# Performance work log

Measured on AMD Instinct MI355X. Metric: run time of the kernel, lower is better.

The kernel has to match this reference:

```python
import jax, jax.numpy as jnp
import numpy as np

HEADS = 8


def setup_inputs() -> dict:
    key = jax.random.key(0)
    k0, k1, k2, k3 = jax.random.split(key, 4)
    N, C_in, T = 4, 256, 2048
    C_kq, C_out = 512, 512
    x = jax.random.normal(k0, (N, C_in, T), dtype=jnp.float32)
    # Conv1d(kernel_size=1, bias=False) weights squeezed to (out, in)
    Wq = jax.random.normal(k1, (C_kq, C_in), dtype=jnp.float32) * 0.02
    Wk = jax.random.normal(k2, (C_kq, C_in), dtype=jnp.float32) * 0.02
    Wv = jax.random.normal(k3, (C_out, C_in), dtype=jnp.float32) * 0.02
    return {"x": x, "Wq": Wq, "Wk": Wk, "Wv": Wv}


def reference(x, Wq, Wk, Wv):
    N, C, T = x.shape
    H = HEADS
    C_kq = Wq.shape[0]
    C_out = Wv.shape[0]
    dk = C_kq // H
    dv = C_out // H
    # 1x1 conv == per-timestep linear projection
    q = jnp.einsum('oc,nct->not', Wq, x).reshape(N, H, dk, T)
    k = jnp.einsum('oc,nct->not', Wk, x).reshape(N, H, dk, T)
    v = jnp.einsum('oc,nct->not', Wv, x).reshape(N, H, dv, T)
    scale = 1.0 / np.sqrt(dk)
    # scores[n,h,tk,tq] = sum_d q[n,h,d,tq] * k[n,h,d,tk]
    scores = jnp.einsum('nhdq,nhdk->nhkq', q, k) * scale
    attn = jax.nn.softmax(scores, axis=2)  # softmax over key axis tk
    # out[n,h,d,tq] = sum_tk attn[n,h,tk,tq] * v[n,h,d,tk]
    out = jnp.einsum('nhkq,nhdk->nhdq', attn, v)
    return out.reshape(N, C_out, T)
```

## Files before the change

kernel.cpp:

```cpp
#include <hip/hip_runtime.h>
#include <stdint.h>

#define T_SEQ 2048
#define CIN 256
#define COUT 512
#define NHEAD 8
#define DH 64
#define LROW 72

typedef __bf16 bf16x8 __attribute__((ext_vector_type(8)));
typedef float f32x4 __attribute__((ext_vector_type(4)));
typedef float f32x16 __attribute__((ext_vector_type(16)));
typedef unsigned short u16x8 __attribute__((ext_vector_type(8)));
typedef unsigned u32x4 __attribute__((ext_vector_type(4)));

static __device__ __forceinline__ unsigned short bf16_rne(float f) {
  unsigned u = __builtin_bit_cast(unsigned, f);
  u += 0x7FFFu + ((u >> 16) & 1u);
  return (unsigned short)(u >> 16);
}

static __device__ __forceinline__ unsigned cvt_pk_bf16(float lo, float hi) {
  unsigned r;
  asm("v_cvt_pk_bf16_f32 %0, %1, %2" : "=v"(r) : "v"(lo), "v"(hi));
  return r;
}

static __device__ __forceinline__ void plswap(unsigned& a, unsigned& b) {
  auto rr = __builtin_amdgcn_permlane32_swap((int)a, (int)b, false, false);
  a = (unsigned)rr[0];
  b = (unsigned)rr[1];
}

static __device__ __forceinline__ bf16x8 ld_frag(const unsigned short* p) {
  u16x8 v = *(const u16x8*)p;
  return __builtin_bit_cast(bf16x8, v);
}

__global__ __launch_bounds__(256) void pack_k(const float* __restrict__ x,
                                              const float* __restrict__ wq,
                                              const float* __restrict__ wk,
                                              const float* __restrict__ wv,
                                              unsigned short* __restrict__ wb,
                                              unsigned short* __restrict__ xT) {
  __shared__ float tile[64][65];
  const int b = blockIdx.x;
  const int i = threadIdx.x;
  if (b < 1536) {
    const int idx = b * 256 + i;
    const float* src = (idx < 131072) ? wq : (idx < 262144) ? wk : wv;
    wb[idx] = bf16_rne(src[idx & 131071]);
    return;
  }
  const int b2 = b - 1536;
  const int t0 = (b2 & 31) * 64, c0 = ((b2 >> 5) & 3) * 64, n = b2 >> 7;
  {
    const int cc = i >> 2, tch = (i & 3) * 16;
    const float* src = x + ((size_t)n * CIN + c0 + cc) * T_SEQ + t0 + tch;
    const float4* s4 = (const float4*)src;
#pragma unroll
    for (int q = 0; q < 4; ++q) {
      float4 v = s4[q];
      tile[cc][tch + q * 4 + 0] = v.x;
      tile[cc][tch + q * 4 + 1] = v.y;
      tile[cc][tch + q * 4 + 2] = v.z;
      tile[cc][tch + q * 4 + 3] = v.w;
    }
  }
  __syncthreads();
  {
    const int tt = i >> 2, cch = (i & 3) * 16;
    unsigned short* dst = xT + ((size_t)n * T_SEQ + t0 + tt) * CIN + c0 + cch;
    u16x8 w0, w1;
#pragma unroll
    for (int j = 0; j < 8; ++j) w0[j] = bf16_rne(tile[cch + j][tt]);
#pragma unroll
    for (int j = 0; j < 8; ++j) w1[j] = bf16_rne(tile[cch + 8 + j][tt]);
    *(u16x8*)dst = w0;
    *(u16x8*)(dst + 8) = w1;
  }
}

__global__ __launch_bounds__(256) void proj_k(const unsigned short* __restrict__ wb,
                                              const unsigned short* __restrict__ xT,
                                              unsigned short* __restrict__ qb,
                                              unsigned short* __restrict__ kb,
                                              unsigned short* __restrict__ vb) {
  __shared__ unsigned short vt_lds[64][136];
  const int n = blockIdx.z;
  const unsigned short* X = xT + (size_t)n * T_SEQ * CIN;
  const int tid = threadIdx.x, wave = tid >> 6, lane = tid & 63;
  const int c = lane & 15, g = lane >> 4;
  const int o0 = blockIdx.x * 64;
  const int t0 = blockIdx.y * 128 + wave * 32;

  bf16x8 a[8][2];
#pragma unroll
  for (int k8 = 0; k8 < 8; ++k8)
#pragma unroll
    for (int mt = 0; mt < 2; ++mt)
      a[k8][mt] = ld_frag(X + (size_t)(t0 + mt * 16 + c) * CIN + k8 * 32 + g * 8);

  const f32x4 z4 = {0.f, 0.f, 0.f, 0.f};
  const int h = o0 >> 6;
  const size_t base = ((size_t)(n * NHEAD + h)) * T_SEQ * DH;

  for (int w = 0; w < 3; ++w) {
    const unsigned short* W = wb + (size_t)w * COUT * CIN;
    f32x4 acc[2][4];
#pragma unroll
    for (int mt = 0; mt < 2; ++mt)
#pragma unroll
      for (int no = 0; no < 4; ++no) acc[mt][no] = z4;

#pragma unroll
    for (int k8 = 0; k8 < 8; ++k8) {
      bf16x8 b[4];
#pragma unroll
      for (int no = 0; no < 4; ++no)
        b[no] = ld_frag(W + (size_t)(o0 + no * 16 + c) * CIN + k8 * 32 + g * 8);
#pragma unroll
      for (int mt = 0; mt < 2; ++mt)
#pragma unroll
        for (int no = 0; no < 4; ++no)
          acc[mt][no] = __builtin_amdgcn_mfma_f32_16x16x32_bf16(a[k8][mt], b[no], acc[mt][no], 0, 0, 0);
    }

    if (w == 2) {
#pragma unroll
      for (int mt = 0; mt < 2; ++mt)
#pragma unroll
        for (int no = 0; no < 4; ++no) {
          const int d = no * 16 + c;
          const int lt = (wave * 32) + mt * 16 + 4 * g;
#pragma unroll
          for (int pr = 0; pr < 2; ++pr) {
            const unsigned pw = (unsigned)bf16_rne(acc[mt][no][2 * pr]) |
                                ((unsigned)bf16_rne(acc[mt][no][2 * pr + 1]) << 16);
            *(unsigned*)&vt_lds[d][lt + 2 * pr] = pw;
          }
        }
      __syncthreads();
      const int row = tid >> 2, seg = tid & 3;
      unsigned short* dst = vb + base + (size_t)row * T_SEQ + blockIdx.y * 128 + seg * 32;
      const unsigned short* srcl = &vt_lds[row][seg * 32];
#pragma unroll
      for (int q = 0; q < 4; ++q) *(u16x8*)(dst + q * 8) = *(const u16x8*)(srcl + q * 8);
    } else {
      unsigned short* dst = (w == 0) ? qb : kb;
      const float scale = (w == 0) ? 0.18033688011112043f : 1.0f;
#pragma unroll
      for (int mt = 0; mt < 2; ++mt)
#pragma unroll
        for (int no = 0; no < 4; ++no)
#pragma unroll
          for (int r = 0; r < 4; ++r) {
            const int t = t0 + mt * 16 + 4 * g + r;
            const int d = no * 16 + c;
            dst[base + (size_t)t * DH + d] = bf16_rne(acc[mt][no][r] * scale);
          }
    }
  }
}

__global__ __launch_bounds__(256) void attn_k(const unsigned short* __restrict__ qb,
                                              const unsigned short* __restrict__ kb,
                                              const unsigned short* __restrict__ vbt,
                                              float* __restrict__ outp) {
  __shared__ unsigned short smem[4 * 4608];
  unsigned short* kA = smem;
  unsigned short* kB = smem + 4608;
  unsigned short* vA = smem + 9216;
  unsigned short* vB = smem + 13824;

  const int bid = blockIdx.x;
  const int sid = (bid & 7) * 32 + (bid >> 3);
  const int tqt = sid & 7, nh = sid >> 3;

  const int tid = threadIdx.x;
  const int lane = tid & 63;
  const int wave = tid >> 6;
  const int ln = lane & 31, hi = lane >> 5;
  const int tq0 = tqt * 256 + wave * 64;
  const unsigned short* Q = qb + (size_t)nh * T_SEQ * DH;
  const unsigned short* K = kb + (size_t)nh * T_SEQ * DH;
  const unsigned short* V = vbt + (size_t)nh * T_SEQ * DH;

  bf16x8 qf0[4], qf1[4];
#pragma unroll
  for (int dblk = 0; dblk < 4; ++dblk) {
    qf0[dblk] = ld_frag(Q + (size_t)(tq0 + ln) * DH + dblk * 16 + hi * 8);
    qf1[dblk] = ld_frag(Q + (size_t)(tq0 + 32 + ln) * DH + dblk * 16 + hi * 8);
  }

  const f32x16 z16 = {0.f, 0.f, 0.f, 0.f, 0.f, 0.f, 0.f, 0.f,
                      0.f, 0.f, 0.f, 0.f, 0.f, 0.f, 0.f, 0.f};
  f32x16 oacc00 = z16, oacc01 = z16, oacc10 = z16, oacc11 = z16;
  float l_run0 = 0.f, l_run1 = 0.f;

  const int srow = tid & 63, sseg = tid >> 6;
  const unsigned short* kseg = K + (size_t)srow * DH + sseg * 16;
  const unsigned short* vseg = V + (size_t)srow * T_SEQ + sseg * 16;
  const int swoff = srow * LROW + sseg * 16;
  const int row0 = ln * LROW;
  const int row1 = (32 + ln) * LROW;
  const int hioff = hi * 8;

  const int NT = T_SEQ / 64;
  u16x8 kn0, kn1, vn0, vn1;

  {
    u16x8 a0 = *(const u16x8*)kseg;
    u16x8 a1 = *(const u16x8*)(kseg + 8);
    u16x8 b0 = *(const u16x8*)vseg;
    u16x8 b1 = *(const u16x8*)(vseg + 8);
    *(u16x8*)&kA[swoff] = a0;
    *(u16x8*)&kA[swoff + 8] = a1;
    *(u16x8*)&vA[swoff] = b0;
    *(u16x8*)&vA[swoff + 8] = b1;
    kn0 = *(const u16x8*)(kseg + 64 * DH);
    kn1 = *(const u16x8*)(kseg + 64 * DH + 8);
  }
  __syncthreads();

  f32x16 sa[4], sb[4];
  {
    __builtin_amdgcn_s_setprio(1);
#pragma unroll
    for (int dblk = 0; dblk < 4; ++dblk) {
      bf16x8 ka0 = ld_frag(kA + row0 + dblk * 16 + hioff);
      bf16x8 ka1 = ld_frag(kA + row1 + dblk * 16 + hioff);
      sa[0] = __builtin_amdgcn_mfma_f32_32x32x16_bf16(ka0, qf0[dblk], (dblk == 0) ? z16 : sa[0], 0, 0, 0);
      sa[1] = __builtin_amdgcn_mfma_f32_32x32x16_bf16(ka1, qf0[dblk], (dblk == 0) ? z16 : sa[1], 0, 0, 0);
      sa[2] = __builtin_amdgcn_mfma_f32_32x32x16_bf16(ka0, qf1[dblk], (dblk == 0) ? z16 : sa[2], 0, 0, 0);
      sa[3] = __builtin_amdgcn_mfma_f32_32x32x16_bf16(ka1, qf1[dblk], (dblk == 0) ? z16 : sa[3], 0, 0, 0);
    }
    __builtin_amdgcn_s_setprio(0);
  }
  *(u16x8*)&kB[swoff] = kn0;
  *(u16x8*)&kB[swoff + 8] = kn1;
  kn0 = *(const u16x8*)(kseg + 2 * 64 * DH);
  kn1 = *(const u16x8*)(kseg + 2 * 64 * DH + 8);
  vn0 = *(const u16x8*)(vseg + 64);
  vn1 = *(const u16x8*)(vseg + 64 + 8);
  __syncthreads();

  auto body = [&](int t, f32x16 (&sc)[4], f32x16 (&sn)[4],
                  unsigned short* krd, unsigned short* kwr,
                  unsigned short* vrd, unsigned short* vwr) {
    const bool qn = (t + 1 < NT);
    if (qn) {
      __builtin_amdgcn_s_setprio(1);
#pragma unroll
      for (int dblk = 0; dblk < 4; ++dblk) {
        bf16x8 ka0 = ld_frag(krd + row0 + dblk * 16 + hioff);
        bf16x8 ka1 = ld_frag(krd + row1 + dblk * 16 + hioff);
        sn[0] = __builtin_amdgcn_mfma_f32_32x32x16_bf16(ka0, qf0[dblk], (dblk == 0) ? z16 : sn[0], 0, 0, 0);
        sn[1] = __builtin_amdgcn_mfma_f32_32x32x16_bf16(ka1, qf0[dblk], (dblk == 0) ? z16 : sn[1], 0, 0, 0);
        sn[2] = __builtin_amdgcn_mfma_f32_32x32x16_bf16(ka0, qf1[dblk], (dblk == 0) ? z16 : sn[2], 0, 0, 0);
        sn[3] = __builtin_amdgcn_mfma_f32_32x32x16_bf16(ka1, qf1[dblk], (dblk == 0) ? z16 : sn[3], 0, 0, 0);
      }
      __builtin_amdgcn_s_setprio(0);
    }
    if (t + 1 < NT) {
      *(u16x8*)&vwr[swoff] = vn0;
      *(u16x8*)&vwr[swoff + 8] = vn1;
    }
    if (t + 2 < NT) {
      *(u16x8*)&kwr[swoff] = kn0;
      *(u16x8*)&kwr[swoff + 8] = kn1;
    }
    if (t + 2 < NT) {
      vn0 = *(const u16x8*)(vseg + (size_t)(t + 2) * 64);
      vn1 = *(const u16x8*)(vseg + (size_t)(t + 2) * 64 + 8);
    }
    if (t + 3 < NT) {
      kn0 = *(const u16x8*)(kseg + (size_t)(t + 3) * (64 * DH));
      kn1 = *(const u16x8*)(kseg + (size_t)(t + 3) * (64 * DH) + 8);
    }
    bf16x8 pa0[4], pa1[4];
    {
      float cs = 0.f;
#pragma unroll
      for (int r = 0; r < 16; ++r) {
        sc[0][r] = __builtin_amdgcn_exp2f(sc[0][r]);
        sc[1][r] = __builtin_amdgcn_exp2f(sc[1][r]);
        cs += sc[0][r] + sc[1][r];
      }
      cs += __shfl_xor(cs, 32);
      l_run0 += cs;
      unsigned W0[8], W1[8];
#pragma unroll
      for (int j = 0; j < 8; ++j) {
        W0[j] = cvt_pk_bf16(sc[0][2 * j], sc[0][2 * j + 1]);
        W1[j] = cvt_pk_bf16(sc[1][2 * j], sc[1][2 * j + 1]);
      }
      plswap(W0[0], W0[2]); plswap(W0[1], W0[3]);
      plswap(W0[4], W0[6]); plswap(W0[5], W0[7]);
      plswap(W1[0], W1[2]); plswap(W1[1], W1[3]);
      plswap(W1[4], W1[6]); plswap(W1[5], W1[7]);
      u32x4 f;
      f[0] = W0[0]; f[1] = W0[1]; f[2] = W0[2]; f[3] = W0[3];
      pa0[0] = __builtin_bit_cast(bf16x8, f);
      f[0] = W0[4]; f[1] = W0[5]; f[2] = W0[6]; f[3] = W0[7];
      pa0[1] = __builtin_bit_cast(bf16x8, f);
      f[0] = W1[0]; f[1] = W1[1]; f[2] = W1[2]; f[3] = W1[3];
      pa0[2] = __builtin_bit_cast(bf16x8, f);
      f[0] = W1[4]; f[1] = W1[5]; f[2] = W1[6]; f[3] = W1[7];
      pa0[3] = __builtin_bit_cast(bf16x8, f);
    }
    {
      float cs = 0.f;
#pragma unroll
      for (int r = 0; r < 16; ++r) {
        sc[2][r] = __builtin_amdgcn_exp2f(sc[2][r]);
        sc[3][r] = __builtin_amdgcn_exp2f(sc[3][r]);
        cs += sc[2][r] + sc[3][r];
      }
      cs += __shfl_xor(cs, 32);
      l_run1 += cs;
      unsigned W0[8], W1[8];
#pragma unroll
      for (int j = 0; j < 8; ++j) {
        W0[j] = cvt_pk_bf16(sc[2][2 * j], sc[2][2 * j + 1]);
        W1[j] = cvt_pk_bf16(sc[3][2 * j], sc[3][2 * j + 1]);
      }
      plswap(W0[0], W0[2]); plswap(W0[1], W0[3]);
      plswap(W0[4], W0[6]); plswap(W0[5], W0[7]);
      plswap(W1[0], W1[2]); plswap(W1[1], W1[3]);
      plswap(W1[4], W1[6]); plswap(W1[5], W1[7]);
      u32x4 f;
      f[0] = W0[0]; f[1] = W0[1]; f[2] = W0[2]; f[3] = W0[3];
      pa1[0] = __builtin_bit_cast(bf16x8, f);
      f[0] = W0[4]; f[1] = W0[5]; f[2] = W0[6]; f[3] = W0[7];
      pa1[1] = __builtin_bit_cast(bf16x8, f);
      f[0] = W1[0]; f[1] = W1[1]; f[2] = W1[2]; f[3] = W1[3];
      pa1[2] = __builtin_bit_cast(bf16x8, f);
      f[0] = W1[4]; f[1] = W1[5]; f[2] = W1[6]; f[3] = W1[7];
      pa1[3] = __builtin_bit_cast(bf16x8, f);
    }
    __builtin_amdgcn_s_setprio(1);
#pragma unroll
    for (int kbk = 0; kbk < 4; ++kbk) {
      bf16x8 vf0 = ld_frag(vrd + row0 + kbk * 16 + hioff);
      bf16x8 vf1 = ld_frag(vrd + row1 + kbk * 16 + hioff);
      oacc00 = __builtin_amdgcn_mfma_f32_32x32x16_bf16(pa0[kbk], vf0, oacc00, 0, 0, 0);
      oacc01 = __builtin_amdgcn_mfma_f32_32x32x16_bf16(pa0[kbk], vf1, oacc01, 0, 0, 0);
      oacc10 = __builtin_amdgcn_mfma_f32_32x32x16_bf16(pa1[kbk], vf0, oacc10, 0, 0, 0);
      oacc11 = __builtin_amdgcn_mfma_f32_32x32x16_bf16(pa1[kbk], vf1, oacc11, 0, 0, 0);
    }
    __builtin_amdgcn_s_setprio(0);
    __syncthreads();
  };

  for (int tt = 0; tt < NT; tt += 2) {
    body(tt, sa, sb, kB, kA, vA, vB);
    body(tt + 1, sb, sa, kA, kB, vB, vA);
  }

  const int n = nh >> 3, h = nh & 7;
  const size_t obase = (size_t)(n * COUT + h * DH) * T_SEQ;
  const int d0 = ln, d1 = 32 + ln;
#pragma unroll
  for (int rq = 0; rq < 4; ++rq) {
    const int tbase = tq0 + 8 * rq + 4 * hi;
    f32x4 o0, o1, o2, o3;
#pragma unroll
    for (int j = 0; j < 4; ++j) {
      const float lv0 = __shfl(l_run0, 8 * rq + 4 * hi + j);
      const float inv0 = __builtin_amdgcn_rcpf(lv0);
      const float lv1 = __shfl(l_run1, 8 * rq + 4 * hi + j);
      const float inv1 = __builtin_amdgcn_rcpf(lv1);
      o0[j] = oacc00[4 * rq + j] * inv0;
      o1[j] = oacc01[4 * rq + j] * inv0;
      o2[j] = oacc10[4 * rq + j] * inv1;
      o3[j] = oacc11[4 * rq + j] * inv1;
    }
    *(f32x4*)&outp[obase + (size_t)d0 * T_SEQ + tbase] = o0;
    *(f32x4*)&outp[obase + (size_t)d1 * T_SEQ + tbase] = o1;
    *(f32x4*)&outp[obase + (size_t)d0 * T_SEQ + tbase + 32] = o2;
    *(f32x4*)&outp[obase + (size_t)d1 * T_SEQ + tbase + 32] = o3;
  }
}

extern "C" void kernel_launch(void* const* d_in, const int* in_sizes, int n_in,
                              void* d_out, int out_size, void* d_ws, size_t ws_size,
                              hipStream_t stream) {
  (void)in_sizes; (void)n_in; (void)out_size; (void)ws_size;
  const float* x  = (const float*)d_in[0];
  const float* Wq = (const float*)d_in[1];
  const float* Wk = (const float*)d_in[2];
  const float* Wv = (const float*)d_in[3];
  float* outp = (float*)d_out;

  char* ws = (char*)d_ws;
  unsigned short* wb = (unsigned short*)ws;
  unsigned short* xT = (unsigned short*)(ws + 786432);
  unsigned short* qb = (unsigned short*)(ws + 4980736);
  unsigned short* kb = qb + 4194304;
  unsigned short* vb = kb + 4194304;

  pack_k<<<2048, 256, 0, stream>>>(x, Wq, Wk, Wv, wb, xT);
  proj_k<<<dim3(8, 16, 4), 256, 0, stream>>>(wb, xT, qb, kb, vb);
  attn_k<<<256, 256, 0, stream>>>(qb, kb, vb, outp);
}
```

Before: 89.94 us.

## Split attention key range across two wave groups per block and merge

Doubles the block to 512 threads, with each half of the waves processing half of the key/value sequence using its own double-buffered LDS tiles. After the loop, the second half writes its output accumulators and row sums to shared memory and the first half adds them before normalizing and storing. This aims to raise per-CU wave occupancy and latency hiding, since the grid has only one block per CU. The cost is more LDS, a reduction step and extra register pressure at 512 threads.

New measurement: 139.9 us. +55.5%, slower.

```diff
diff --git a/kernel.cpp b/kernel.cpp
--- a/kernel.cpp
+++ b/kernel.cpp
@@ -163,25 +163,22 @@
   }
 }
 
-__global__ __launch_bounds__(256) void attn_k(const unsigned short* __restrict__ qb,
+__global__ __launch_bounds__(512) void attn_k(const unsigned short* __restrict__ qb,
                                               const unsigned short* __restrict__ kb,
                                               const unsigned short* __restrict__ vbt,
                                               float* __restrict__ outp) {
-  __shared__ unsigned short smem[4 * 4608];
-  unsigned short* kA = smem;
-  unsigned short* kB = smem + 4608;
-  unsigned short* vA = smem + 9216;
-  unsigned short* vB = smem + 13824;
+  __shared__ unsigned short smem[2 * 4 * 4608];
 
   const int bid = blockIdx.x;
   const int sid = (bid & 7) * 32 + (bid >> 3);
   const int tqt = sid & 7, nh = sid >> 3;
 
   const int tid = threadIdx.x;
-  const int lane = tid & 63;
-  const int wave = tid >> 6;
+  const int wave = tid >> 6, lane = tid & 63;
+  const int half = wave >> 2;
+  const int wq4 = wave & 3;
   const int ln = lane & 31, hi = lane >> 5;
-  const int tq0 = tqt * 256 + wave * 64;
+  const int tq0 = tqt * 256 + wq4 * 64;
   const unsigned short* Q = qb + (size_t)nh * T_SEQ * DH;
   const unsigned short* K = kb + (size_t)nh * T_SEQ * DH;
   const unsigned short* V = vbt + (size_t)nh * T_SEQ * DH;
@@ -195,18 +192,25 @@
 
   const f32x16 z16 = {0.f, 0.f, 0.f, 0.f, 0.f, 0.f, 0.f, 0.f,
                       0.f, 0.f, 0.f, 0.f, 0.f, 0.f, 0.f, 0.f};
-  f32x16 oacc00 = z16, oacc01 = z16, oacc10 = z16, oacc11 = z16;
+  f32x16 oacc00 = z16, oacc01 = z16;
+  f32x16 oacc10 = z16, oacc11 = z16;
   float l_run0 = 0.f, l_run1 = 0.f;
 
-  const int srow = tid & 63, sseg = tid >> 6;
-  const unsigned short* kseg = K + (size_t)srow * DH + sseg * 16;
-  const unsigned short* vseg = V + (size_t)srow * T_SEQ + sseg * 16;
+  const int ht = tid & 255;
+  const int srow = ht & 63, sseg = ht >> 6;
+  const unsigned short* kseg = K + (size_t)(half * 1024 + srow) * DH + sseg * 16;
+  const unsigned short* vseg = V + (size_t)srow * T_SEQ + half * 1024 + sseg * 16;
   const int swoff = srow * LROW + sseg * 16;
   const int row0 = ln * LROW;
   const int row1 = (32 + ln) * LROW;
   const int hioff = hi * 8;
 
-  const int NT = T_SEQ / 64;
+  unsigned short* kA = smem + half * 18432;
+  unsigned short* kB = kA + 4608;
+  unsigned short* vA = kA + 9216;
+  unsigned short* vB = kA + 13824;
+
+  const int NT2 = T_SEQ / 64 / 2;
   u16x8 kn0, kn1, vn0, vn1;
 
   {
@@ -239,8 +243,8 @@
   }
   *(u16x8*)&kB[swoff] = kn0;
   *(u16x8*)&kB[swoff + 8] = kn1;
-  kn0 = *(const u16x8*)(kseg + 2 * 64 * DH);
-  kn1 = *(const u16x8*)(kseg + 2 * 64 * DH + 8);
+  kn0 = *(const u16x8*)(kseg + 2 * (size_t)(64 * DH));
+  kn1 = *(const u16x8*)(kseg + 2 * (size_t)(64 * DH) + 8);
   vn0 = *(const u16x8*)(vseg + 64);
   vn1 = *(const u16x8*)(vseg + 64 + 8);
   __syncthreads();
@@ -248,8 +252,7 @@
   auto body = [&](int t, f32x16 (&sc)[4], f32x16 (&sn)[4],
                   unsigned short* krd, unsigned short* kwr,
                   unsigned short* vrd, unsigned short* vwr) {
-    const bool qn = (t + 1 < NT);
-    if (qn) {
+    if (t + 1 < NT2) {
       __builtin_amdgcn_s_setprio(1);
 #pragma unroll
       for (int dblk = 0; dblk < 4; ++dblk) {
@@ -262,19 +265,19 @@
       }
       __builtin_amdgcn_s_setprio(0);
     }
-    if (t + 1 < NT) {
+    if (t + 1 < NT2) {
       *(u16x8*)&vwr[swoff] = vn0;
       *(u16x8*)&vwr[swoff + 8] = vn1;
     }
-    if (t + 2 < NT) {
+    if (t + 2 < NT2) {
       *(u16x8*)&kwr[swoff] = kn0;
       *(u16x8*)&kwr[swoff + 8] = kn1;
     }
-    if (t + 2 < NT) {
+    if (t + 2 < NT2) {
       vn0 = *(const u16x8*)(vseg + (size_t)(t + 2) * 64);
       vn1 = *(const u16x8*)(vseg + (size_t)(t + 2) * 64 + 8);
     }
-    if (t + 3 < NT) {
+    if (t + 3 < NT2) {
       kn0 = *(const u16x8*)(kseg + (size_t)(t + 3) * (64 * DH));
       kn1 = *(const u16x8*)(kseg + (size_t)(t + 3) * (64 * DH) + 8);
     }
@@ -353,33 +356,63 @@
     __syncthreads();
   };
 
-  for (int tt = 0; tt < NT; tt += 2) {
+  for (int tt = 0; tt < NT2; tt += 2) {
     body(tt, sa, sb, kB, kA, vA, vB);
     body(tt + 1, sb, sa, kA, kB, vB, vA);
   }
 
-  const int n = nh >> 3, h = nh & 7;
-  const size_t obase = (size_t)(n * COUT + h * DH) * T_SEQ;
-  const int d0 = ln, d1 = 32 + ln;
-#pragma unroll
-  for (int rq = 0; rq < 4; ++rq) {
-    const int tbase = tq0 + 8 * rq + 4 * hi;
-    f32x4 o0, o1, o2, o3;
-#pragma unroll
-    for (int j = 0; j < 4; ++j) {
-      const float lv0 = __shfl(l_run0, 8 * rq + 4 * hi + j);
-      const float inv0 = __builtin_amdgcn_rcpf(lv0);
-      const float lv1 = __shfl(l_run1, 8 * rq + 4 * hi + j);
-      const float inv1 = __builtin_amdgcn_rcpf(lv1);
-      o0[j] = oacc00[4 * rq + j] * inv0;
-      o1[j] = oacc01[4 * rq + j] * inv0;
-      o2[j] = oacc10[4 * rq + j] * inv1;
-      o3[j] = oacc11[4 * rq + j] * inv1;
-    }
-    *(f32x4*)&outp[obase + (size_t)d0 * T_SEQ + tbase] = o0;
-    *(f32x4*)&outp[obase + (size_t)d1 * T_SEQ + tbase] = o1;
-    *(f32x4*)&outp[obase + (size_t)d0 * T_SEQ + tbase + 32] = o2;
-    *(f32x4*)&outp[obase + (size_t)d1 * T_SEQ + tbase + 32] = o3;
+  float* mbuf = (float*)smem;
+  const int MS = 4224;
+  if (half == 1) {
+    float* mb = mbuf + wq4 * MS;
+#pragma unroll
+    for (int r = 0; r < 16; ++r) mb[r * 64 + lane] = oacc00[r];
+#pragma unroll
+    for (int r = 0; r < 16; ++r) mb[1024 + r * 64 + lane] = oacc01[r];
+#pragma unroll
+    for (int r = 0; r < 16; ++r) mb[2048 + r * 64 + lane] = oacc10[r];
+#pragma unroll
+    for (int r = 0; r < 16; ++r) mb[3072 + r * 64 + lane] = oacc11[r];
+    mb[4096 + lane] = l_run0;
+    mb[4160 + lane] = l_run1;
+  }
+  __syncthreads();
+  if (half == 0) {
+    float* mb = mbuf + wq4 * MS;
+#pragma unroll
+    for (int r = 0; r < 16; ++r) oacc00[r] += mb[r * 64 + lane];
+#pragma unroll
+    for (int r = 0; r < 16; ++r) oacc01[r] += mb[1024 + r * 64 + lane];
+#pragma unroll
+    for (int r = 0; r < 16; ++r) oacc10[r] += mb[2048 + r * 64 + lane];
+#pragma unroll
+    for (int r = 0; r < 16; ++r) oacc11[r] += mb[3072 + r * 64 + lane];
+    l_run0 += mb[4096 + lane];
+    l_run1 += mb[4160 + lane];
+
+    const int n = nh >> 3, h = nh & 7;
+    const size_t obase = (size_t)(n * COUT + h * DH) * T_SEQ;
+    const int d0 = ln, d1 = 32 + ln;
+#pragma unroll
+    for (int rq = 0; rq < 4; ++rq) {
+      const int tbase = tq0 + 8 * rq + 4 * hi;
+      f32x4 o0, o1, o2, o3;
+#pragma unroll
+      for (int j = 0; j < 4; ++j) {
+        const float lv0 = __shfl(l_run0, 8 * rq + 4 * hi + j);
+        const float inv0 = __builtin_amdgcn_rcpf(lv0);
+        const float lv1 = __shfl(l_run1, 8 * rq + 4 * hi + j);
+        const float inv1 = __builtin_amdgcn_rcpf(lv1);
+        o0[j] = oacc00[4 * rq + j] * inv0;
+        o1[j] = oacc01[4 * rq + j] * inv0;
+        o2[j] = oacc10[4 * rq + j] * inv1;
+        o3[j] = oacc11[4 * rq + j] * inv1;
+      }
+      *(f32x4*)&outp[obase + (size_t)d0 * T_SEQ + tbase] = o0;
+      *(f32x4*)&outp[obase + (size_t)d1 * T_SEQ + tbase] = o1;
+      *(f32x4*)&outp[obase + (size_t)d0 * T_SEQ + tbase + 32] = o2;
+      *(f32x4*)&outp[obase + (size_t)d1 * T_SEQ + tbase + 32] = o3;
+    }
   }
 }
 
@@ -402,5 +435,5 @@
 
   pack_k<<<2048, 256, 0, stream>>>(x, Wq, Wk, Wv, wb, xT);
   proj_k<<<dim3(8, 16, 4), 256, 0, stream>>>(wb, xT, qb, kb, vb);
-  attn_k<<<256, 256, 0, stream>>>(qb, kb, vb, outp);
-}
+  attn_k<<<256, 512, 0, stream>>>(qb, kb, vb, outp);
+}
```
